# Kernel optimization log

Hardware: AMD Instinct MI355X
Metric: run time of the kernel (lower is better)

## Reference

```python
import jax, jax.numpy as jnp
import numpy as np

K = 4        # num_kernels
TOPK = 16    # per-row hyperedge sparsification
CHEB_T = 2   # Chebyshev order
ROW_TEMP = 1.0
PI_ITERS = 5  # power-iteration steps


def setup_inputs() -> dict:
    key = jax.random.key(0)
    N, D, D_out = 4096, 256, 256
    ks = jax.random.split(key, 5)
    X = jax.random.normal(ks[0], (N, D), jnp.float32)
    L_k = jax.random.normal(ks[1], (K, D, D), jnp.float32) * 0.02
    alpha = jnp.ones((K,), jnp.float32)
    theta = jax.random.normal(ks[2], (CHEB_T + 1, D), jnp.float32) * 0.02
    rho_raw = jnp.zeros((), jnp.float32)
    proj_w = jax.random.normal(ks[3], (D_out, D), jnp.float32) / np.sqrt(D).astype(np.float32)
    proj_b = jnp.zeros((D_out,), jnp.float32)
    return {"X": X, "L_k": L_k, "alpha": alpha, "theta": theta,
            "rho_raw": rho_raw, "proj_w": proj_w, "proj_b": proj_b}


def reference(X, L_k, alpha, theta, rho_raw, proj_w, proj_b):
    N, D = X.shape
    tau = max(ROW_TEMP, 1e-6)
    # 1) K bilinear kernels: A_k = X L_k X^T / sqrt(D), row-softmax with temp
    A = jnp.einsum('nd,kde,me->knm', X, L_k, X) / jnp.sqrt(jnp.asarray(D, X.dtype))
    H_stack = jax.nn.softmax(A / tau, axis=2)                 # (K, N, N)
    w = jax.nn.softmax(alpha)[:, None, None]
    H_fused = (H_stack * w).sum(0)                            # (N, N)
    # 2) incidence B (N, E=K*N): hyperedge (k,i) holds topk targets of row i of head k
    vals, idx = jax.lax.top_k(H_stack, TOPK)                  # (K, N, TOPK)
    vals = vals / (vals.sum(-1, keepdims=True) + 1e-9)
    E = K * N
    cols = jnp.arange(K)[:, None, None] * N + jnp.arange(N)[None, :, None]
    cols = jnp.broadcast_to(cols, (K, N, TOPK)).reshape(-1)
    rows = idx.reshape(-1)
    B = jnp.zeros((N, E), X.dtype).at[rows, cols].set(vals.reshape(-1))
    W = jnp.ones((E,), X.dtype)
    # 3) normalized hypergraph Laplacian L = I - Dv^{-1/2} B W De^{-1} B^T Dv^{-1/2}
    De = B.sum(0) + 1e-9                                      # (E,)
    Dv = (B * W[None, :]).sum(1) + 1e-9                       # (N,)
    Dv_is = jnp.sqrt(1.0 / Dv)
    S = (B * (W / De)[None, :]) @ B.T                         # (N, N)
    S_norm = Dv_is[:, None] * S * Dv_is[None, :]
    I = jnp.eye(N, dtype=X.dtype)
    L = I - S_norm
    # 4) lambda_max via power iteration on detached L (constant w.r.t. grads)
    Ld = jax.lax.stop_gradient(L)
    v = jax.random.normal(jax.random.key(1), (N, 1), X.dtype)
    v = v / (jnp.linalg.norm(v) + 1e-9)
    for _ in range(PI_ITERS):
        v = Ld @ v
        v = v / (jnp.linalg.norm(v) + 1e-9)
    lam = jnp.clip((v.T @ (Ld @ v)).squeeze(), 1e-3, None)
    lam = jax.lax.stop_gradient(lam)
    L_tilde = (2.0 / lam) * L - I
    # Chebyshev recursion: sum_t T_t(L_tilde) X * theta_t, then ELU
    T0 = X
    out = T0 * theta[0][None, :]
    T1 = L_tilde @ X
    out = out + T1 * theta[1][None, :]
    for t in range(2, CHEB_T + 1):
        T2 = 2.0 * (L_tilde @ T1) - T0
        out = out + T2 * theta[t][None, :]
        T0, T1 = T1, T2
    Z_spec = jax.nn.elu(out)
    # 5) residual blend with kernel diffusion
    Z_kern = H_fused @ X
    rho = jax.nn.sigmoid(rho_raw)
    Z_mix = rho * Z_spec + (1.0 - rho) * Z_kern
    # 6) final projection
    return Z_mix @ proj_w.T + proj_b
```

## Files before the change

kernel.cpp:

```cpp
#include <hip/hip_runtime.h>

typedef unsigned short u16;
typedef unsigned long long u64;
typedef _Float16 h16;
typedef __attribute__((ext_vector_type(8))) _Float16 h16x8;
typedef __attribute__((ext_vector_type(4))) _Float16 h16x4;
typedef __attribute__((ext_vector_type(4))) float f32x4;

__device__ __forceinline__ float b2f(u16 u) {
  unsigned x = ((unsigned)u) << 16;
  return __uint_as_float(x);
}
__device__ __forceinline__ unsigned fkey(float f) {
  unsigned b = __float_as_uint(f);
  return (b & 0x80000000u) ? ~b : (b | 0x80000000u);
}
__device__ __forceinline__ float unfkey(unsigned u) {
  unsigned b = (u & 0x80000000u) ? (u ^ 0x80000000u) : ~u;
  return __uint_as_float(b);
}
__device__ __forceinline__ f32x4 mfma16(h16x8 a, h16x8 b, f32x4 c) {
  return __builtin_amdgcn_mfma_f32_16x16x32_f16(a, b, c, 0, 0, 0);
}
__device__ __forceinline__ void gl_lds16(const void* g, void* l) {
  __builtin_amdgcn_global_load_lds(
      (const __attribute__((address_space(1))) unsigned*)g,
      (__attribute__((address_space(3))) unsigned*)l, 16, 0, 0);
}
__device__ __forceinline__ u64 wave_max_u64(u64 k) {
#pragma unroll
  for (int off = 32; off; off >>= 1) {
    u64 o = __shfl_xor(k, off);
    if (o > k) k = o;
  }
  return k;
}
__device__ __forceinline__ float cvt_in(const void* p, int i, int f) {
  return f ? ((const float*)p)[i] : b2f(((const u16*)p)[i]);
}

__device__ __forceinline__ int detect_f32_local(const u16* __restrict__ X) {
  __shared__ int dcnt;
  if (threadIdx.x == 0) dcnt = 0;
  __syncthreads();
  int sane = 0;
  for (int j = threadIdx.x; j < 4096; j += blockDim.x) {
    u16 u = X[j * 2];
    int e = (u >> 7) & 0xff;
    if (u == 0 || (e >= 112 && e <= 142)) sane++;
  }
  atomicAdd(&dcnt, sane);
  __syncthreads();
  return (dcnt < 3072) ? 1 : 0;
}

__global__ __launch_bounds__(256) void split_input3(
    const void* __restrict__ in, h16* __restrict__ hi, h16* __restrict__ lo,
    float* __restrict__ f32out, int n) {
  int f = detect_f32_local((const u16*)in);
  int stride = gridDim.x * 256;
  for (int i = blockIdx.x * 256 + threadIdx.x; i < n; i += stride) {
    float x = cvt_in(in, i, f);
    h16 h = (h16)x;
    hi[i] = h;
    lo[i] = (h16)(x - (float)h);
    if (f32out) f32out[i] = x;
  }
}

__global__ __launch_bounds__(256) void split_LW(
    const void* __restrict__ Xin, const void* __restrict__ Lin,
    h16* __restrict__ Lhi, h16* __restrict__ Llo, const void* __restrict__ Win,
    h16* __restrict__ Whi, h16* __restrict__ Wlo) {
  int f = detect_f32_local((const u16*)Xin);
  int tid = threadIdx.x;
  if (blockIdx.x < 256) {
#pragma unroll
    for (int j = 0; j < 4; ++j) {
      int i = blockIdx.x * 1024 + j * 256 + tid;
      float x = cvt_in(Lin, i, f);
      h16 h = (h16)x;
      Lhi[i] = h;
      Llo[i] = (h16)(x - (float)h);
    }
  } else {
    int b = blockIdx.x - 256;
#pragma unroll
    for (int j = 0; j < 4; ++j) {
      int i = b * 1024 + j * 256 + tid;
      float x = cvt_in(Win, i, f);
      h16 h = (h16)x;
      Whi[i] = h;
      Wlo[i] = (h16)(x - (float)h);
    }
  }
}

__global__ __launch_bounds__(1024) void prep_small(
    const void* __restrict__ Xin, const void* __restrict__ theta,
    const void* __restrict__ bpin, const void* __restrict__ alpha,
    const void* __restrict__ rho_raw, float* __restrict__ thetaf,
    float* __restrict__ biasf, float* __restrict__ scal) {
  int f = detect_f32_local((const u16*)Xin);
  int tid = threadIdx.x;
  if (tid < 768)
    thetaf[tid] = cvt_in(theta, tid, f);
  else if (tid < 1024)
    biasf[tid - 768] = cvt_in(bpin, tid - 768, f);
  if (tid == 0) {
    float a[4], e[4], m = -1e30f, s = 0.f;
    for (int i = 0; i < 4; ++i) {
      a[i] = cvt_in(alpha, i, f);
      m = fmaxf(m, a[i]);
    }
    for (int i = 0; i < 4; ++i) { e[i] = expf(a[i] - m); s += e[i]; }
    for (int i = 0; i < 4; ++i) scal[i] = e[i] / s;
    float rr = cvt_in(rho_raw, 0, f);
    scal[4] = 1.f / (1.f + expf(-rr));
  }
}

template <bool BIAS, bool SPLITOUT>
__global__ __launch_bounds__(256) void gemm3_nt(
    const h16* __restrict__ Ah, const h16* __restrict__ Al,
    const h16* __restrict__ Bh, const h16* __restrict__ Bl,
    float* __restrict__ C, h16* __restrict__ Yh, h16* __restrict__ Yl,
    const float* __restrict__ bias, float alpha, int M, int Nc, int Kd,
    long batchA, long batchB, long batchC) {
  const h16* Abh = Ah + (size_t)blockIdx.z * batchA;
  const h16* Abl = Al + (size_t)blockIdx.z * batchA;
  const h16* Bbh = Bh + (size_t)blockIdx.z * batchB;
  const h16* Bbl = Bl + (size_t)blockIdx.z * batchB;
  int bn = blockIdx.x, bm = blockIdx.y;
  int tid = threadIdx.x;
  int wid = tid >> 6, lane = tid & 63;
  __shared__ h16 Ash[64 * 40], Asl[64 * 40], Bsh[64 * 40], Bsl[64 * 40];
  f32x4 acc00 = {}, acc01 = {}, acc10 = {}, acc11 = {};
  int lr = tid >> 2;
  int lc = (tid & 3) << 3;
  size_t aoff = (size_t)(bm * 64 + lr) * Kd + lc;
  size_t boff = (size_t)(bn * 64 + lr) * Kd + lc;
  int wm = (wid & 1) * 32, wn = (wid >> 1) * 32;
  int fr = lane & 15;
  int fc = (lane >> 4) << 3;
  for (int k0 = 0; k0 < Kd; k0 += 32) {
    uint4 avh = *(const uint4*)(Abh + aoff + k0);
    uint4 avl = *(const uint4*)(Abl + aoff + k0);
    uint4 bvh = *(const uint4*)(Bbh + boff + k0);
    uint4 bvl = *(const uint4*)(Bbl + boff + k0);
    __syncthreads();
    *(uint4*)(Ash + lr * 40 + lc) = avh;
    *(uint4*)(Asl + lr * 40 + lc) = avl;
    *(uint4*)(Bsh + lr * 40 + lc) = bvh;
    *(uint4*)(Bsl + lr * 40 + lc) = bvl;
    __syncthreads();
    h16x8 a0h = *(const h16x8*)(Ash + (wm + fr) * 40 + fc);
    h16x8 a1h = *(const h16x8*)(Ash + (wm + 16 + fr) * 40 + fc);
    h16x8 b0h = *(const h16x8*)(Bsh + (wn + fr) * 40 + fc);
    h16x8 b1h = *(const h16x8*)(Bsh + (wn + 16 + fr) * 40 + fc);
    h16x8 a0l = *(const h16x8*)(Asl + (wm + fr) * 40 + fc);
    h16x8 a1l = *(const h16x8*)(Asl + (wm + 16 + fr) * 40 + fc);
    h16x8 b0l = *(const h16x8*)(Bsl + (wn + fr) * 40 + fc);
    h16x8 b1l = *(const h16x8*)(Bsl + (wn + 16 + fr) * 40 + fc);
    acc00 = mfma16(a0h, b0h, acc00);
    acc01 = mfma16(a0h, b1h, acc01);
    acc10 = mfma16(a1h, b0h, acc10);
    acc11 = mfma16(a1h, b1h, acc11);
    acc00 = mfma16(a0h, b0l, acc00);
    acc01 = mfma16(a0h, b1l, acc01);
    acc10 = mfma16(a1h, b0l, acc10);
    acc11 = mfma16(a1h, b1l, acc11);
    acc00 = mfma16(a0l, b0h, acc00);
    acc01 = mfma16(a0l, b1h, acc01);
    acc10 = mfma16(a1l, b0h, acc10);
    acc11 = mfma16(a1l, b1h, acc11);
  }
  int crow = (lane >> 4) << 2;
  int ccol = lane & 15;
  f32x4 accs[2][2] = {{acc00, acc01}, {acc10, acc11}};
#pragma unroll
  for (int i = 0; i < 2; ++i)
#pragma unroll
    for (int j = 0; j < 2; ++j) {
      int r0 = bm * 64 + wm + 16 * i + crow;
      int c0 = bn * 64 + wn + 16 * j + ccol;
#pragma unroll
      for (int rg = 0; rg < 4; ++rg) {
        size_t off = (size_t)(r0 + rg) * Nc + c0;
        float v = accs[i][j][rg] * alpha;
        if constexpr (SPLITOUT) {
          h16* Yhb = Yh + (size_t)blockIdx.z * batchC;
          h16* Ylb = Yl + (size_t)blockIdx.z * batchC;
          h16 hh = (h16)v;
          Yhb[off] = hh;
          Ylb[off] = (h16)(v - (float)hh);
        } else {
          if constexpr (BIAS) v += bias[c0];
          float* Cb = C + (size_t)blockIdx.z * batchC;
          Cb[off] = v;
        }
      }
    }
}

__global__ __launch_bounds__(256) void gemm3_big(
    const h16* __restrict__ Ah, const h16* __restrict__ Al,
    const h16* __restrict__ Bh, const h16* __restrict__ Bl,
    float* __restrict__ C, float alpha, int M, int Nc, int Kd) {
  __shared__ h16 sAh[128 * 32], sAl[128 * 32], sBh[128 * 32], sBl[128 * 32];
  int tid = threadIdx.x, wid = tid >> 6, lane = tid & 63;
  int bm = blockIdx.y, bn = blockIdx.x;
  int srow = 32 * wid + (lane >> 2);
  int scnk = lane & 3;
  int fr = lane & 15, fcc = lane >> 4;
  f32x4 acc[4][4] = {};
  const h16* gA[2] = {Ah, Al};
  const h16* gB[2] = {Bh, Bl};
  h16* sA[2] = {sAh, sAl};
  h16* sB[2] = {sBh, sBl};
  int wm = (wid & 1) * 64, wn = (wid >> 1) * 64;
  for (int k0 = 0; k0 < Kd; k0 += 32) {
    __syncthreads();
#pragma unroll
    for (int h = 0; h < 2; ++h) {
      int r = srow + 16 * h;
      int cs = scnk ^ ((r >> 1) & 3);
      size_t goffA = (size_t)(bm * 128 + r) * Kd + k0 + cs * 8;
      size_t goffB = (size_t)(bn * 128 + r) * Kd + k0 + cs * 8;
      int loff = (32 * wid + 16 * h) * 32;
#pragma unroll
      for (int p = 0; p < 2; ++p) {
        gl_lds16(gA[p] + goffA, sA[p] + loff);
        gl_lds16(gB[p] + goffB, sB[p] + loff);
      }
    }
    __syncthreads();
    h16x8 fa[2][4], fb[2][4];
#pragma unroll
    for (int i = 0; i < 4; ++i) {
      int ra = wm + 16 * i + fr;
      int ca = (fcc ^ ((ra >> 1) & 3)) * 8;
      fa[0][i] = *(const h16x8*)(sAh + ra * 32 + ca);
      fa[1][i] = *(const h16x8*)(sAl + ra * 32 + ca);
      int rb = wn + 16 * i + fr;
      int cb = (fcc ^ ((rb >> 1) & 3)) * 8;
      fb[0][i] = *(const h16x8*)(sBh + rb * 32 + cb);
      fb[1][i] = *(const h16x8*)(sBl + rb * 32 + cb);
    }
#pragma unroll
    for (int i = 0; i < 4; ++i)
#pragma unroll
      for (int j = 0; j < 4; ++j) {
        acc[i][j] = mfma16(fa[0][i], fb[0][j], acc[i][j]);
        acc[i][j] = mfma16(fa[0][i], fb[1][j], acc[i][j]);
        acc[i][j] = mfma16(fa[1][i], fb[0][j], acc[i][j]);
      }
  }
  int crow = (lane >> 4) << 2, ccol = lane & 15;
#pragma unroll
  for (int i = 0; i < 4; ++i)
#pragma unroll
    for (int j = 0; j < 4; ++j) {
      int r0 = bm * 128 + wm + 16 * i + crow;
      int c0 = bn * 128 + wn + 16 * j + ccol;
#pragma unroll
      for (int rg = 0; rg < 4; ++rg)
        C[(size_t)(r0 + rg) * Nc + c0] = acc[i][j][rg] * alpha;
    }
}

__global__ __launch_bounds__(256) void gemm_ks4(
    const h16* __restrict__ Eall, const h16* __restrict__ B,
    float* __restrict__ Cpart) {
  __shared__ h16 sA[128 * 32], sB[128 * 32];
  int tid = threadIdx.x, wid = tid >> 6, lane = tid & 63;
  int bm = blockIdx.y, bn = blockIdx.x, zz = blockIdx.z;
  int head = zz >> 2, kz = zz & 3;
  const h16* A = Eall + (size_t)head * 4096 * 4096;
  int kbase = kz * 1024;
  int srow = 32 * wid + (lane >> 2);
  int scnk = lane & 3;
  int fr = lane & 15, fcc = lane >> 4;
  f32x4 acc[4][4] = {};
  int wm = (wid & 1) * 64, wn = (wid >> 1) * 64;
  for (int k0 = 0; k0 < 1024; k0 += 32) {
    __syncthreads();
#pragma unroll
    for (int h = 0; h < 2; ++h) {
      int r = srow + 16 * h;
      int cs = scnk ^ ((r >> 1) & 3);
      size_t goffA = (size_t)(bm * 128 + r) * 4096 + kbase + k0 + cs * 8;
      size_t goffB = (size_t)(bn * 128 + r) * 4096 + kbase + k0 + cs * 8;
      int loff = (32 * wid + 16 * h) * 32;
      gl_lds16(A + goffA, sA + loff);
      gl_lds16(B + goffB, sB + loff);
    }
    __syncthreads();
    h16x8 fa[4], fb[4];
#pragma unroll
    for (int i = 0; i < 4; ++i) {
      int ra = wm + 16 * i + fr;
      int ca = (fcc ^ ((ra >> 1) & 3)) * 8;
      fa[i] = *(const h16x8*)(sA + ra * 32 + ca);
      int rb = wn + 16 * i + fr;
      int cb = (fcc ^ ((rb >> 1) & 3)) * 8;
      fb[i] = *(const h16x8*)(sB + rb * 32 + cb);
    }
#pragma unroll
    for (int i = 0; i < 4; ++i)
#pragma unroll
      for (int j = 0; j < 4; ++j)
        acc[i][j] = mfma16(fa[i], fb[j], acc[i][j]);
  }
  float* Cp = Cpart + (size_t)zz * 4096 * 256;
  int crow = (lane >> 4) << 2, ccol = lane & 15;
#pragma unroll
  for (int i = 0; i < 4; ++i)
#pragma unroll
    for (int j = 0; j < 4; ++j) {
      int r0 = bm * 128 + wm + 16 * i + crow;
      int c0 = bn * 128 + wn + 16 * j + ccol;
#pragma unroll
      for (int rg = 0; rg < 4; ++rg)
        Cp[(size_t)(r0 + rg) * 256 + c0] = acc[i][j][rg];
    }
}

__global__ __launch_bounds__(256) void ksred_hist(
    const float* __restrict__ Cpart, const float* __restrict__ scal,
    const float* __restrict__ rowSinv, float* __restrict__ Zk,
    const float* __restrict__ topv, const int* __restrict__ topi,
    int* __restrict__ pCnt, float* __restrict__ pDv,
    float* __restrict__ DeIS) {
  __shared__ int lc[4096];
  __shared__ float ld[4096];
  int tid = threadIdx.x;
  if (blockIdx.x < 1024) {
    int i = (blockIdx.x * 256 + tid) * 4;
    int row = i >> 8;
    float4 out = {0.f, 0.f, 0.f, 0.f};
#pragma unroll
    for (int k = 0; k < 4; ++k) {
      float4 s = {0.f, 0.f, 0.f, 0.f};
#pragma unroll
      for (int z = 0; z < 4; ++z) {
        float4 p =
            *(const float4*)(Cpart + (size_t)(k * 4 + z) * 4096 * 256 + i);
        s.x += p.x; s.y += p.y; s.z += p.z; s.w += p.w;
      }
      float sc = scal[k] * rowSinv[k * 4096 + row];
      out.x += sc * s.x; out.y += sc * s.y;
      out.z += sc * s.z; out.w += sc * s.w;
    }
    *(float4*)(Zk + i) = out;
  } else {
    int b = blockIdx.x - 1024;
    for (int j = tid; j < 4096; j += 256) { lc[j] = 0; ld[j] = 0.f; }
    __syncthreads();
    int base = b * 4096;
#pragma unroll
    for (int j = 0; j < 16; ++j) {
      int t = base + j * 256 + tid;
      atomicAdd(&lc[topi[t]], 1);
      atomicAdd(&ld[topi[t]], topv[t]);
    }
    __syncthreads();
    for (int j = tid; j < 4096; j += 256) {
      pCnt[base + j] = lc[j];
      pDv[base + j] = ld[j];
    }
    int e = b * 256 + tid;
    const float4* p = (const float4*)(topv + ((size_t)e << 4));
    float4 a = p[0], bb = p[1], c = p[2], d = p[3];
    float s = ((a.x + a.y) + (a.z + a.w)) + ((bb.x + bb.y) + (bb.z + bb.w)) +
              ((c.x + c.y) + (c.z + c.w)) + ((d.x + d.y) + (d.z + d.w));
    DeIS[e] = 1.0f / sqrtf(s + 1e-9f);
  }
}

__global__ __launch_bounds__(256) void transpose16(
    const u16* __restrict__ in, u16* __restrict__ out, int rows, int cols) {
  __shared__ u16 t[32][33];
  const u16* ib = in + (size_t)blockIdx.z * rows * cols;
  u16* ob = out + (size_t)blockIdx.z * rows * cols;
  int r0 = blockIdx.x * 32, c0 = blockIdx.y * 32;
  int tx = threadIdx.x & 31, ty = threadIdx.x >> 5;
#pragma unroll
  for (int i = 0; i < 32; i += 8)
    t[ty + i][tx] = ib[(size_t)(r0 + ty + i) * cols + c0 + tx];
  __syncthreads();
#pragma unroll
  for (int i = 0; i < 32; i += 8)
    ob[(size_t)(c0 + ty + i) * rows + r0 + tx] = t[tx][ty + i];
}

__global__ __launch_bounds__(256) void row_softmax_topk(
    const float* __restrict__ A, float* __restrict__ topv,
    int* __restrict__ topi, h16* __restrict__ E, float* __restrict__ rowSinvK,
    int khead) {
  __shared__ u64 candK[4][256];
  __shared__ int candN[4];
  int wid = threadIdx.x >> 6, lane = threadIdx.x & 63;
  int row = blockIdx.x * 4 + wid;
  const float* arow = A + ((size_t)row << 12);
  if (lane == 0) candN[wid] = 0;
  __syncthreads();
  float lm = -INFINITY;
#pragma unroll
  for (int t = 0; t < 16; ++t) {
    float4 v = *(const float4*)(arow + (t << 8) + (lane << 2));
    lm = fmaxf(lm, fmaxf(fmaxf(v.x, v.y), fmaxf(v.z, v.w)));
  }
  float m = lm;
#pragma unroll
  for (int off = 32; off; off >>= 1) m = fmaxf(m, __shfl_xor(m, off));
  u64 lk = ((u64)fkey(lm) << 32) | (unsigned)lane;
  float T = 0.f;
  for (int r = 0; r < 16; ++r) {
    u64 k2 = wave_max_u64(lk);
    if (lk == k2) lk = 0;
    if (r == 15) T = unfkey((unsigned)(k2 >> 32));
  }
  h16* erow = E + ((size_t)row << 12);
  int* cn = &candN[wid];
  u64* ck = candK[wid];
  float s = 0.f;
  for (int t = 0; t < 16; ++t) {
    int c = (t << 8) + (lane << 2);
    float4 v = *(const float4*)(arow + c);
    float e0 = __expf(v.x - m), e1 = __expf(v.y - m);
    float e2 = __expf(v.z - m), e3 = __expf(v.w - m);
    s += (e0 + e1) + (e2 + e3);
    h16x4 hv = {(h16)e0, (h16)e1, (h16)e2, (h16)e3};
    *(h16x4*)(erow + c) = hv;
    if (v.x >= T) {
      int sl = atomicAdd(cn, 1);
      if (sl < 256) ck[sl] = ((u64)fkey(v.x) << 32) | (unsigned)(~(unsigned)c);
    }
    if (v.y >= T) {
      int sl = atomicAdd(cn, 1);
      if (sl < 256) ck[sl] = ((u64)fkey(v.y) << 32) | (unsigned)(~(unsigned)(c + 1));
    }
    if (v.z >= T) {
      int sl = atomicAdd(cn, 1);
      if (sl < 256) ck[sl] = ((u64)fkey(v.z) << 32) | (unsigned)(~(unsigned)(c + 2));
    }
    if (v.w >= T) {
      int sl = atomicAdd(cn, 1);
      if (sl < 256) ck[sl] = ((u64)fkey(v.w) << 32) | (unsigned)(~(unsigned)(c + 3));
    }
  }
#pragma unroll
  for (int off = 32; off; off >>= 1) s += __shfl_xor(s, off);
  if (lane == 0) rowSinvK[row] = 1.f / s;
  __syncthreads();
  int cnt = min(*cn, 256);
  u64 loc[4] = {0ull, 0ull, 0ull, 0ull};
  int nl = 0;
  for (int j = lane; j < cnt; j += 64)
    if (nl < 4) loc[nl++] = ck[j];
#define CSW(a, b)                     \
  {                                   \
    if (loc[b] > loc[a]) {            \
      u64 tt = loc[a];                \
      loc[a] = loc[b];                \
      loc[b] = tt;                    \
    }                                 \
  }
  CSW(0, 1) CSW(2, 3) CSW(0, 2) CSW(1, 3) CSW(1, 2)
#undef CSW
  float myv = 0.f;
  int myi = 0;
  float sum16 = 0.f;
  for (int r = 0; r < 16; ++r) {
    u64 key = loc[0];
    u64 k2 = wave_max_u64(key);
    float wv = unfkey((unsigned)(k2 >> 32));
    int wi = (int)(~(unsigned)(k2 & 0xffffffffu));
    if (key == k2 && key != 0ull) {
      loc[0] = loc[1];
      loc[1] = loc[2];
      loc[2] = loc[3];
      loc[3] = 0ull;
    }
    sum16 += expf(wv - m);
    if (r == lane) { myv = wv; myi = wi; }
  }
  if (lane < 16) {
    size_t o = (((size_t)khead << 12) + row) * 16 + lane;
    topv[o] = expf(myv - m) / (sum16 + 1e-9f * s);
    topi[o] = myi;
  }
}

__global__ __launch_bounds__(256) void col_scan(
    const int* __restrict__ pCnt, const float* __restrict__ pDv,
    int* __restrict__ cnt, float* __restrict__ Dvis,
    int* __restrict__ blockBase, float* __restrict__ v0) {
  int i = blockIdx.x * 256 + threadIdx.x;
  int run = 0;
  float dv = 0.f;
#pragma unroll
  for (int b = 0; b < 64; ++b) {
    blockBase[b * 4096 + i] = run;
    run += pCnt[b * 4096 + i];
    dv += pDv[b * 4096 + i];
  }
  cnt[i] = run;
  Dvis[i] = sqrtf(1.0f / (dv + 1e-9f));
  {
    int tid = i;
    unsigned j = (unsigned)(tid & 2047);
    unsigned x0 = j, x1 = j + 2048u;
    const unsigned ks0 = 0u, ks1 = 1u, ks2 = 0x1BD11BDAu;
#define TF_R(r)                                \
    {                                          \
      x0 += x1;                                \
      x1 = (x1 << (r)) | (x1 >> (32 - (r)));   \
      x1 ^= x0;                                \
    }
    x0 += ks0; x1 += ks1;
    TF_R(13) TF_R(15) TF_R(26) TF_R(6)  x0 += ks1; x1 += ks2 + 1u;
    TF_R(17) TF_R(29) TF_R(16) TF_R(24) x0 += ks2; x1 += ks0 + 2u;
    TF_R(13) TF_R(15) TF_R(26) TF_R(6)  x0 += ks0; x1 += ks1 + 3u;
    TF_R(17) TF_R(29) TF_R(16) TF_R(24) x0 += ks1; x1 += ks2 + 4u;
    TF_R(13) TF_R(15) TF_R(26) TF_R(6)  x0 += ks2; x1 += ks0 + 5u;
#undef TF_R
    unsigned bits = (tid < 2048) ? x0 : x1;
    float u01 = __uint_as_float((bits >> 9) | 0x3f800000u) - 1.0f;
    const float lo = -0.99999994f;
    float u = fmaxf(lo, u01 * 2.0f + lo);
    float w = -log1pf(-u * u);
    float p;
    if (w < 5.0f) {
      float t = w - 2.5f;
      p = 2.81022636e-08f;
      p = 3.43273939e-07f + p * t;
      p = -3.5233877e-06f + p * t;
      p = -4.39150654e-06f + p * t;
      p = 0.00021858087f + p * t;
      p = -0.00125372503f + p * t;
      p = -0.00417768164f + p * t;
      p = 0.246640727f + p * t;
      p = 1.50140941f + p * t;
    } else {
      float t = sqrtf(w) - 3.0f;
      p = -0.000200214257f;
      p = 0.000100950558f + p * t;
      p = 0.00134934322f + p * t;
      p = -0.00367342844f + p * t;
      p = 0.00573950773f + p * t;
      p = -0.0076224613f + p * t;
      p = 0.00943887047f + p * t;
      p = 1.00167406f + p * t;
      p = 2.83297682f + p * t;
    }
    v0[tid] = 1.41421354f * (p * u);
  }
}

__global__ __launch_bounds__(256) void scan_rowptr(const int* __restrict__ cnt,
                                                   int* __restrict__ rowptr) {
  __shared__ int part[256];
  int tid = threadIdx.x;
  int base = tid * 16;
  int loc[16];
  int s = 0;
#pragma unroll
  for (int j = 0; j < 16; ++j) { loc[j] = s; s += cnt[base + j]; }
  part[tid] = s;
  __syncthreads();
  for (int off = 1; off < 256; off <<= 1) {
    int v = (tid >= off) ? part[tid - off] : 0;
    __syncthreads();
    part[tid] += v;
    __syncthreads();
  }
  int pre = (tid == 0) ? 0 : part[tid - 1];
#pragma unroll
  for (int j = 0; j < 16; ++j) rowptr[base + j] = pre + loc[j];
  if (tid == 255) rowptr[4096] = part[255];
}

__global__ __launch_bounds__(256) void csr_fill3(
    const float* __restrict__ topv, const int* __restrict__ topi,
    const float* __restrict__ Dvis, const float* __restrict__ DeIS,
    const int* __restrict__ rowptr, const int* __restrict__ blockBase,
    float* __restrict__ cvals, int* __restrict__ colE,
    float* __restrict__ cvalR) {
  __shared__ int lcur[4096];
  int tid = threadIdx.x, b = blockIdx.x;
  int base = b * 4096;
  for (int j = tid; j < 4096; j += 256)
    lcur[j] = rowptr[j] + blockBase[base + j];
  __syncthreads();
#pragma unroll
  for (int j = 0; j < 16; ++j) {
    int t = base + j * 256 + tid;
    int i = topi[t];
    int e = t >> 4;
    float c = Dvis[i] * topv[t] * DeIS[e];
    cvals[t] = c;
    int slot = atomicAdd(&lcur[i], 1);
    colE[slot] = e;
    cvalR[slot] = c;
  }
}

__global__ __launch_bounds__(256) void spmv_edge(
    const float* __restrict__ cvals, const int* __restrict__ topi,
    const float* __restrict__ v, float* __restrict__ g) {
  int e = blockIdx.x * 256 + threadIdx.x;
  float acc = 0.f;
#pragma unroll
  for (int p = 0; p < 16; ++p)
    acc += cvals[e * 16 + p] * v[topi[e * 16 + p]];
  g[e] = acc;
}

__global__ __launch_bounds__(256) void spmv_row(
    const int* __restrict__ rowptr, const int* __restrict__ colE,
    const float* __restrict__ cvalR, const float* __restrict__ g,
    const float* __restrict__ vin, float* __restrict__ vout) {
  int wid = threadIdx.x >> 6, lane = threadIdx.x & 63;
  int row = blockIdx.x * 4 + wid;
  int s = rowptr[row], e = rowptr[row + 1];
  float acc = 0.f;
  for (int j = s + lane; j < e; j += 64) acc += cvalR[j] * g[colE[j]];
#pragma unroll
  for (int off = 32; off; off >>= 1) acc += __shfl_xor(acc, off);
  if (lane == 0) vout[row] = vin[row] - acc;
}

__global__ __launch_bounds__(256) void pi_dots(const float* __restrict__ w5,
                                               const float* __restrict__ w6,
                                               float* __restrict__ scal) {
  __shared__ float r1[256], r2[256];
  int tid = threadIdx.x;
  float a = 0.f, b = 0.f;
  for (int i = tid; i < 4096; i += 256) {
    float x = w5[i];
    a += x * x;
    b += x * w6[i];
  }
  r1[tid] = a; r2[tid] = b;
  __syncthreads();
  for (int off = 128; off; off >>= 1) {
    if (tid < off) { r1[tid] += r1[tid + off]; r2[tid] += r2[tid + off]; }
    __syncthreads();
  }
  if (tid == 0) scal[5] = fmaxf(r2[0] / r1[0], 1e-3f);
}

__global__ __launch_bounds__(256) void spmm_edge(
    const float* __restrict__ cvals, const int* __restrict__ topi,
    const float* __restrict__ M, float* __restrict__ G) {
  int wid = threadIdx.x >> 6, lane = threadIdx.x & 63;
  int e = blockIdx.x * 4 + wid;
  int cb = lane << 2;
  const float* cv = cvals + ((size_t)e << 4);
  const int* ti = topi + ((size_t)e << 4);
  float cc[16];
  int ix[16];
#pragma unroll
  for (int p = 0; p < 16; ++p) { cc[p] = cv[p]; ix[p] = ti[p]; }
  float4 acc[4] = {};
#pragma unroll
  for (int h = 0; h < 2; ++h) {
    float4 g[8];
#pragma unroll
    for (int p = 0; p < 8; ++p)
      g[p] = *(const float4*)(M + ((size_t)ix[h * 8 + p] << 8) + cb);
#pragma unroll
    for (int p = 0; p < 8; ++p) {
      float c = cc[h * 8 + p];
      float4 gg = g[p];
      int a = p & 3;
      acc[a].x += c * gg.x; acc[a].y += c * gg.y;
      acc[a].z += c * gg.z; acc[a].w += c * gg.w;
    }
  }
  float4 r;
  r.x = (acc[0].x + acc[1].x) + (acc[2].x + acc[3].x);
  r.y = (acc[0].y + acc[1].y) + (acc[2].y + acc[3].y);
  r.z = (acc[0].z + acc[1].z) + (acc[2].z + acc[3].z);
  r.w = (acc[0].w + acc[1].w) + (acc[2].w + acc[3].w);
  *(float4*)(G + ((size_t)e << 8) + cb) = r;
}

template <int MODE>
__global__ __launch_bounds__(256) void spmm_row_ep(
    const int* __restrict__ rowptr, const int* __restrict__ colE,
    const float* __restrict__ cvalR, const float* __restrict__ G,
    const float* __restrict__ Xf, float* __restrict__ T1,
    const float* __restrict__ Zk, const float* __restrict__ thetaf,
    const float* __restrict__ scal, h16* __restrict__ Zmh,
    h16* __restrict__ Zml) {
  int wid = threadIdx.x >> 6, lane = threadIdx.x & 63;
  int row = blockIdx.x * 4 + wid;
  int cb = lane << 2;
  int s = rowptr[row], e = rowptr[row + 1];
  float4 acc[4] = {};
  int j = s;
  for (; j + 8 <= e; j += 8) {
    int ix[8];
    float cc[8];
#pragma unroll
    for (int t = 0; t < 8; ++t) { ix[t] = colE[j + t]; cc[t] = cvalR[j + t]; }
    float4 g[8];
#pragma unroll
    for (int t = 0; t < 8; ++t)
      g[t] = *(const float4*)(G + ((size_t)ix[t] << 8) + cb);
#pragma unroll
    for (int t = 0; t < 8; ++t) {
      float c = cc[t];
      float4 gg = g[t];
      int a = t & 3;
      acc[a].x += c * gg.x; acc[a].y += c * gg.y;
      acc[a].z += c * gg.z; acc[a].w += c * gg.w;
    }
  }
  for (; j < e; ++j) {
    float c = cvalR[j];
    float4 gg = *(const float4*)(G + ((size_t)colE[j] << 8) + cb);
    acc[0].x += c * gg.x; acc[0].y += c * gg.y;
    acc[0].z += c * gg.z; acc[0].w += c * gg.w;
  }
  float4 z;
  z.x = (acc[0].x + acc[1].x) + (acc[2].x + acc[3].x);
  z.y = (acc[0].y + acc[1].y) + (acc[2].y + acc[3].y);
  z.z = (acc[0].z + acc[1].z) + (acc[2].z + acc[3].z);
  z.w = (acc[0].w + acc[1].w) + (acc[2].w + acc[3].w);
  size_t o = ((size_t)row << 8) + cb;
  float c1 = 2.0f / scal[5];
  float4 x = *(const float4*)(Xf + o);
  if constexpr (MODE == 1) {
    float4 t1;
    t1.x = (c1 - 1.0f) * x.x - c1 * z.x;
    t1.y = (c1 - 1.0f) * x.y - c1 * z.y;
    t1.z = (c1 - 1.0f) * x.z - c1 * z.z;
    t1.w = (c1 - 1.0f) * x.w - c1 * z.w;
    *(float4*)(T1 + o) = t1;
  } else {
    float rho = scal[4];
    float4 t1 = *(const float4*)(T1 + o);
    float4 zk = *(const float4*)(Zk + o);
    h16x4 hh, hl;
#pragma unroll
    for (int q = 0; q < 4; ++q) {
      float xv = (&x.x)[q], t1v = (&t1.x)[q], zv = (&z.x)[q], zkv = (&zk.x)[q];
      int d = cb + q;
      float t2 = 2.0f * ((c1 - 1.0f) * t1v - c1 * zv) - xv;
      float oo = xv * thetaf[d] + t1v * thetaf[256 + d] + t2 * thetaf[512 + d];
      float zs = oo > 0.0f ? oo : expm1f(oo);
      float zm = rho * zs + (1.0f - rho) * zkv;
      h16 h = (h16)zm;
      hh[q] = h;
      hl[q] = (h16)(zm - (float)h);
    }
    *(h16x4*)(Zmh + o) = hh;
    *(h16x4*)(Zml + o) = hl;
  }
}

extern "C" void kernel_launch(void* const* d_in, const int* in_sizes, int n_in,
                              void* d_out, int out_size, void* d_ws,
                              size_t ws_size, hipStream_t stream) {
  (void)in_sizes; (void)n_in; (void)out_size;
  const void* Xin = d_in[0];
  const void* Lin = d_in[1];
  const void* alpha = d_in[2];
  const void* theta = d_in[3];
  const void* rho_raw = d_in[4];
  const void* Wpin = d_in[5];
  const void* bpin = d_in[6];
  float* out = (float*)d_out;

  char* base = (char*)d_ws;
  size_t off = 0;
  auto alloc = [&](size_t bytes) -> char* {
    char* p = base + off;
    off += (bytes + 255) & ~(size_t)255;
    return p;
  };
  float* Abuf = (float*)alloc((size_t)4096 * 4096 * 4);
  h16* Eall = (h16*)alloc((size_t)4 * 4096 * 4096 * 2);
  h16* Yhi = (h16*)alloc((size_t)4 * 4096 * 256 * 2);
  h16* Ylo = (h16*)alloc((size_t)4 * 4096 * 256 * 2);
  h16* Xhi = (h16*)alloc((size_t)4096 * 256 * 2);
  h16* Xlo = (h16*)alloc((size_t)4096 * 256 * 2);
  float* Xf = (float*)alloc((size_t)4096 * 256 * 4);
  h16* XT = (h16*)alloc((size_t)256 * 4096 * 2);
  h16* Lhi = (h16*)alloc((size_t)4 * 256 * 256 * 2);
  h16* Llo = (h16*)alloc((size_t)4 * 256 * 256 * 2);
  h16* LThi = (h16*)alloc((size_t)4 * 256 * 256 * 2);
  h16* LTlo = (h16*)alloc((size_t)4 * 256 * 256 * 2);
  h16* Whi = (h16*)alloc((size_t)256 * 256 * 2);
  h16* Wlo = (h16*)alloc((size_t)256 * 256 * 2);
  float* Zk = (float*)alloc((size_t)4096 * 256 * 4);
  float* T1 = (float*)alloc((size_t)4096 * 256 * 4);
  h16* Zmh = (h16*)alloc((size_t)4096 * 256 * 2);
  h16* Zml = (h16*)alloc((size_t)4096 * 256 * 2);
  float* topv = (float*)alloc((size_t)4 * 4096 * 16 * 4);
  int* topi = (int*)alloc((size_t)4 * 4096 * 16 * 4);
  float* cvals = (float*)alloc((size_t)262144 * 4);
  int* colE = (int*)alloc((size_t)262144 * 4);
  float* cvalR = (float*)alloc((size_t)262144 * 4);
  int* pCnt = (int*)alloc((size_t)64 * 4096 * 4);
  float* pDv = (float*)alloc((size_t)64 * 4096 * 4);
  int* blockBase = (int*)alloc((size_t)64 * 4096 * 4);
  int* rowptr = (int*)alloc(4097 * 4);
  int* cnt = (int*)alloc(4096 * 4);
  float* Dvis = (float*)alloc(4096 * 4);
  float* DeIS = (float*)alloc(16384 * 4);
  float* gE = (float*)alloc(16384 * 4);
  float* wA = (float*)alloc(4096 * 4);
  float* wB = (float*)alloc(4096 * 4);
  float* rowSinv = (float*)alloc((size_t)4 * 4096 * 4);
  float* thetaf = (float*)alloc(768 * 4);
  float* biasf = (float*)alloc(256 * 4);
  float* scal = (float*)alloc(256);
  if (off > ws_size) return;
  float* Kpart = Abuf;
  float* G = Abuf;

  split_input3<<<1024, 256, 0, stream>>>(Xin, Xhi, Xlo, Xf, 4096 * 256);
  split_LW<<<320, 256, 0, stream>>>(Xin, Lin, Lhi, Llo, Wpin, Whi, Wlo);
  prep_small<<<1, 1024, 0, stream>>>(Xin, theta, bpin, alpha, rho_raw, thetaf,
                                     biasf, scal);
  transpose16<<<dim3(128, 8, 1), 256, 0, stream>>>((const u16*)Xhi, (u16*)XT,
                                                   4096, 256);
  transpose16<<<dim3(8, 8, 8), 256, 0, stream>>>((const u16*)Lhi, (u16*)LThi,
                                                 256, 256);
  gemm3_nt<false, true><<<dim3(4, 64, 4), 256, 0, stream>>>(
      Xhi, Xlo, LThi, LTlo, nullptr, Yhi, Ylo, nullptr, 1.0f, 4096, 256, 256,
      0L, 256L * 256L, 4096L * 256L);
  for (int k = 0; k < 4; ++k) {
    gemm3_big<<<dim3(32, 32), 256, 0, stream>>>(
        Yhi + (size_t)k * 4096 * 256, Ylo + (size_t)k * 4096 * 256, Xhi, Xlo,
        Abuf, 0.0625f, 4096, 4096, 256);
    row_softmax_topk<<<1024, 256, 0, stream>>>(
        Abuf, topv, topi, Eall + (size_t)k * 4096 * 4096, rowSinv + k * 4096,
        k);
  }
  gemm_ks4<<<dim3(2, 32, 16), 256, 0, stream>>>(Eall, XT, Kpart);
  ksred_hist<<<1088, 256, 0, stream>>>(Kpart, scal, rowSinv, Zk, topv, topi,
                                       pCnt, pDv, DeIS);
  col_scan<<<16, 256, 0, stream>>>(pCnt, pDv, cnt, Dvis, blockBase, wA);
  scan_rowptr<<<1, 256, 0, stream>>>(cnt, rowptr);
  csr_fill3<<<64, 256, 0, stream>>>(topv, topi, Dvis, DeIS, rowptr, blockBase,
                                    cvals, colE, cvalR);
  for (int it = 0; it < 6; ++it) {
    const float* vi = (it & 1) ? wB : wA;
    float* vo = (it & 1) ? wA : wB;
    spmv_edge<<<64, 256, 0, stream>>>(cvals, topi, vi, gE);
    spmv_row<<<1024, 256, 0, stream>>>(rowptr, colE, cvalR, gE, vi, vo);
  }
  pi_dots<<<1, 256, 0, stream>>>(wB, wA, scal);
  spmm_edge<<<4096, 256, 0, stream>>>(cvals, topi, Xf, G);
  spmm_row_ep<1><<<1024, 256, 0, stream>>>(rowptr, colE, cvalR, G, Xf, T1,
                                           nullptr, thetaf, scal, nullptr,
                                           nullptr);
  spmm_edge<<<4096, 256, 0, stream>>>(cvals, topi, T1, G);
  spmm_row_ep<2><<<1024, 256, 0, stream>>>(rowptr, colE, cvalR, G, Xf, T1, Zk,
                                           thetaf, scal, Zmh, Zml);
  gemm3_nt<true, false><<<dim3(4, 64, 1), 256, 0, stream>>>(
      Zmh, Zml, Whi, Wlo, out, nullptr, nullptr, biasf, 1.0f, 4096, 256, 256,
      0L, 0L, 0L);
}
```

Baseline: 675.8 us.

## Double-buffer gemm_ks4 LDS and retile to 64x256 blocks

The split-K GEMM over the softmax heads now uses 64-row by full-256-column tiles, so each block reads its slice of the large fp16 E matrix only once instead of twice. It also double-buffers the shared-memory staging, so the next K-slab loads while MFMAs run on the current one, removing one barrier per iteration. The grid shrinks from 1024 to 1024 blocks of a different shape (64x16). The cost is more LDS per block (40KB) and more B-operand reloads, since B is small.

```diff
diff --git a/kernel.cpp b/kernel.cpp
--- a/kernel.cpp
+++ b/kernel.cpp
@@ -272,54 +272,70 @@
 __global__ __launch_bounds__(256) void gemm_ks4(
     const h16* __restrict__ Eall, const h16* __restrict__ B,
     float* __restrict__ Cpart) {
-  __shared__ h16 sA[128 * 32], sB[128 * 32];
+  __shared__ h16 sA[2][64 * 32];
+  __shared__ h16 sB[2][256 * 32];
   int tid = threadIdx.x, wid = tid >> 6, lane = tid & 63;
-  int bm = blockIdx.y, bn = blockIdx.x, zz = blockIdx.z;
+  int bm = blockIdx.x, zz = blockIdx.y;
   int head = zz >> 2, kz = zz & 3;
-  const h16* A = Eall + (size_t)head * 4096 * 4096;
-  int kbase = kz * 1024;
-  int srow = 32 * wid + (lane >> 2);
+  const h16* A =
+      Eall + (size_t)head * 4096 * 4096 + (size_t)(bm * 64) * 4096 + kz * 1024;
+  const h16* Bb = B + kz * 1024;
+  int r16 = lane >> 2;
   int scnk = lane & 3;
   int fr = lane & 15, fcc = lane >> 4;
+  int wn = wid * 64;
   f32x4 acc[4][4] = {};
-  int wm = (wid & 1) * 64, wn = (wid >> 1) * 64;
-  for (int k0 = 0; k0 < 1024; k0 += 32) {
-    __syncthreads();
-#pragma unroll
-    for (int h = 0; h < 2; ++h) {
-      int r = srow + 16 * h;
+
+  auto stage = [&](int buf, int k0) {
+    {
+      int r = 16 * wid + r16;
       int cs = scnk ^ ((r >> 1) & 3);
-      size_t goffA = (size_t)(bm * 128 + r) * 4096 + kbase + k0 + cs * 8;
-      size_t goffB = (size_t)(bn * 128 + r) * 4096 + kbase + k0 + cs * 8;
-      int loff = (32 * wid + 16 * h) * 32;
-      gl_lds16(A + goffA, sA + loff);
-      gl_lds16(B + goffB, sB + loff);
-    }
-    __syncthreads();
+      gl_lds16(A + (size_t)r * 4096 + k0 + cs * 8, &sA[buf][(16 * wid) * 32]);
+    }
+#pragma unroll
+    for (int p = 0; p < 4; ++p) {
+      int r = 64 * p + 16 * wid + r16;
+      int cs = scnk ^ ((r >> 1) & 3);
+      gl_lds16(Bb + (size_t)r * 4096 + k0 + cs * 8,
+               &sB[buf][(64 * p + 16 * wid) * 32]);
+    }
+  };
+  auto compute = [&](int buf) {
     h16x8 fa[4], fb[4];
 #pragma unroll
     for (int i = 0; i < 4; ++i) {
-      int ra = wm + 16 * i + fr;
+      int ra = 16 * i + fr;
       int ca = (fcc ^ ((ra >> 1) & 3)) * 8;
-      fa[i] = *(const h16x8*)(sA + ra * 32 + ca);
+      fa[i] = *(const h16x8*)(&sA[buf][ra * 32 + ca]);
       int rb = wn + 16 * i + fr;
       int cb = (fcc ^ ((rb >> 1) & 3)) * 8;
-      fb[i] = *(const h16x8*)(sB + rb * 32 + cb);
+      fb[i] = *(const h16x8*)(&sB[buf][rb * 32 + cb]);
     }
 #pragma unroll
     for (int i = 0; i < 4; ++i)
 #pragma unroll
       for (int j = 0; j < 4; ++j)
         acc[i][j] = mfma16(fa[i], fb[j], acc[i][j]);
-  }
+  };
+
+  stage(0, 0);
+  __syncthreads();
+  for (int t = 0; t < 31; ++t) {
+    int cur = t & 1;
+    stage(cur ^ 1, (t + 1) * 32);
+    compute(cur);
+    __syncthreads();
+  }
+  compute(1);
+
   float* Cp = Cpart + (size_t)zz * 4096 * 256;
   int crow = (lane >> 4) << 2, ccol = lane & 15;
 #pragma unroll
   for (int i = 0; i < 4; ++i)
 #pragma unroll
     for (int j = 0; j < 4; ++j) {
-      int r0 = bm * 128 + wm + 16 * i + crow;
-      int c0 = bn * 128 + wn + 16 * j + ccol;
+      int r0 = bm * 64 + 16 * i + crow;
+      int c0 = wn + 16 * j + ccol;
 #pragma unroll
       for (int rg = 0; rg < 4; ++rg)
         Cp[(size_t)(r0 + rg) * 256 + c0] = acc[i][j][rg];
@@ -843,7 +859,7 @@
         Abuf, topv, topi, Eall + (size_t)k * 4096 * 4096, rowSinv + k * 4096,
         k);
   }
-  gemm_ks4<<<dim3(2, 32, 16), 256, 0, stream>>>(Eall, XT, Kpart);
+  gemm_ks4<<<dim3(64, 16), 256, 0, stream>>>(Eall, XT, Kpart);
   ksred_hist<<<1088, 256, 0, stream>>>(Kpart, scal, rowSinv, Zk, topv, topi,
                                        pCnt, pDv, DeIS);
   col_scan<<<16, 256, 0, stream>>>(pCnt, pDv, cnt, Dvis, blockBase, wA);
```

New measurement: 672.3 us. About the same (-0.5%).
